# Kernel optimization log

Measured on AMD Instinct MI355X. Metric: run time of the kernel, lower is better.

The kernel has to match this reference:

```python
import jax, jax.numpy as jnp
import numpy as np

M, N_ATOMS, E_MOL, IN_CH, OUT_CH = 10000, 32, 64, 64, 128
HID = 2 * OUT_CH  # 256
E_KG = 320000


def gcn_conv(x, edge_index, W, b):
    # PyG GCNConv: out = D^-1/2 (A+I) D^-1/2 (x W) + b
    N = x.shape[0]
    loops = jnp.arange(N)
    src = jnp.concatenate([edge_index[0], loops])
    dst = jnp.concatenate([edge_index[1], loops])
    deg = jax.ops.segment_sum(jnp.ones_like(dst, dtype=x.dtype), dst, num_segments=N)
    dinv = jnp.where(deg > 0, jax.lax.rsqrt(deg), 0.0)
    norm = dinv[src] * dinv[dst]  # [E+N]
    xw = x @ W  # [N, F_out]
    out = jax.ops.segment_sum(xw[src] * norm[:, None], dst, num_segments=N)
    return out + b


def mol_gnn(mx, mei, W1, b1, W2, b2, W3, b3):
    h = jax.nn.relu(gcn_conv(mx, mei, W1, b1))
    h = jax.nn.relu(gcn_conv(h, mei, W2, b2))
    h = gcn_conv(h, mei, W3, b3)
    return jnp.min(h, axis=0)  # torch.min(dim=0).values


def _glorot(key, shape):
    fan_in, fan_out = shape
    s = jnp.sqrt(6.0 / (fan_in + fan_out))
    return jax.random.uniform(key, shape, jnp.float32, -s, s)


def setup_inputs() -> dict:
    key = jax.random.key(0)
    ks = jax.random.split(key, 16)
    mol_x = jax.random.normal(ks[0], (M, N_ATOMS, IN_CH), jnp.float32)
    mol_edge_index = jax.random.randint(ks[1], (M, 2, E_MOL), 0, N_ATOMS, jnp.int64)
    kg_edge_index = jax.random.randint(ks[2], (2, E_KG), 0, M, jnp.int64)
    return {
        "mol_x": mol_x,
        "mol_edge_index": mol_edge_index,
        "kg_edge_index": kg_edge_index,
        "W1": _glorot(ks[3], (IN_CH, HID)), "b1": jnp.zeros((HID,), jnp.float32),
        "W2": _glorot(ks[4], (HID, HID)), "b2": jnp.zeros((HID,), jnp.float32),
        "W3": _glorot(ks[5], (HID, OUT_CH)), "b3": jnp.zeros((OUT_CH,), jnp.float32),
        "Wk1": _glorot(ks[6], (OUT_CH, HID)), "bk1": jnp.zeros((HID,), jnp.float32),
        "Wk2": _glorot(ks[7], (HID, OUT_CH)), "bk2": jnp.zeros((OUT_CH,), jnp.float32),
    }


def reference(mol_x, mol_edge_index, kg_edge_index, W1, b1, W2, b2, W3, b3, Wk1, bk1, Wk2, bk2):
    # Per-molecule GNN + min-pool, vectorized over the M molecules (each graph is disjoint,
    # so vmap == the original per-graph Python loop)
    embed = jax.vmap(mol_gnn, in_axes=(0, 0, None, None, None, None, None, None))(
        mol_x, mol_edge_index, W1, b1, W2, b2, W3, b3)  # [M, OUT_CH]
    h = jax.nn.relu(gcn_conv(embed, kg_edge_index, Wk1, bk1))
    return gcn_conv(h, kg_edge_index, Wk2, bk2)  # [M, OUT_CH]
```

## Files before the change

kernel.cpp:

```cpp
#include <hip/hip_runtime.h>

#define M_MOLS  10000
#define NA      32
#define E_MOL   64
#define IN_CH   64
#define OUT_CH  128
#define HID     256
#define E_KG    320000
#define KG_N    10000

typedef __attribute__((ext_vector_type(8))) short  s16x8;
typedef __attribute__((ext_vector_type(4))) short  s16x4;
typedef __attribute__((ext_vector_type(4))) float  f32x4;

static __device__ __forceinline__ short f2bf(float f) {
    unsigned u = __float_as_uint(f);
    u += 0x7FFFu + ((u >> 16) & 1u);
    return (short)(u >> 16);
}

__global__ void prep_wt(const float* __restrict__ W, short* __restrict__ WT,
                        int K, int C, int total) {
    int idx = blockIdx.x * 256 + threadIdx.x;
    if (idx < total) {
        int c = idx / K, k = idx - c * K;
        WT[idx] = f2bf(W[k * C + c]);
    }
}

__global__ __launch_bounds__(256, 6) void mol_kernel(
    const float* __restrict__ mol_x, const int* __restrict__ mol_ei,
    const short* __restrict__ WT1, const float* __restrict__ b1,
    const short* __restrict__ WT2, const float* __restrict__ b2,
    const short* __restrict__ WT3, const float* __restrict__ b3,
    float* __restrict__ embed)
{
    __shared__ short Hs[NA * HID];
    __shared__ short BT[NA * 40];
    __shared__ float Bm[NA * NA];
    __shared__ float bias_s[2 * HID + OUT_CH];
    __shared__ int   se[E_MOL], de[E_MOL];
    __shared__ float dinv[NA];
    __shared__ int   deg[NA];

    const int t    = threadIdx.x;
    const int mol  = blockIdx.x;
    const int lane = t & 63;
    const int wid  = t >> 6;
    const int lr   = lane & 15;
    const int lk   = lane >> 4;
    char* HsB = (char*)Hs;

    {
        const float4* src = (const float4*)(mol_x + (size_t)mol * (NA * IN_CH));
        float4 a = src[t * 2], b = src[t * 2 + 1];
        s16x8 v;
        v[0] = f2bf(a.x); v[1] = f2bf(a.y); v[2] = f2bf(a.z); v[3] = f2bf(a.w);
        v[4] = f2bf(b.x); v[5] = f2bf(b.y); v[6] = f2bf(b.z); v[7] = f2bf(b.w);
        int row = t >> 3, k0 = (t & 7) * 8;
        int byte = (row << 9) + (k0 << 1); byte ^= (row & 7) << 4;
        *(s16x8*)(HsB + byte) = v;
    }
    {
        const int* eb = mol_ei + (size_t)mol * (2 * E_MOL);
        if (t < E_MOL)            se[t]         = eb[t];
        else if (t < 2 * E_MOL)   de[t - E_MOL] = eb[t];
    }
    if (t < NA) deg[t] = 1;
    for (int i = t; i < NA * NA; i += 256) Bm[i] = 0.f;
    for (int i = t; i < 2 * HID + OUT_CH; i += 256)
        bias_s[i] = (i < HID) ? b1[i] : (i < 2 * HID) ? b2[i - HID] : b3[i - 2 * HID];
    __syncthreads();
    if (t < E_MOL) atomicAdd(&deg[de[t]], 1);
    __syncthreads();
    if (t < NA) dinv[t] = rsqrtf((float)deg[t]);
    __syncthreads();
    if (t < E_MOL) {
        atomicAdd(&Bm[se[t] * NA + de[t]], dinv[se[t]] * dinv[de[t]]);
    } else if (t < E_MOL + NA) {
        int i = t - E_MOL;
        atomicAdd(&Bm[i * NA + i], dinv[i] * dinv[i]);
    }
    __syncthreads();
    for (int i = t; i < NA * NA; i += 256) {
        int r = i >> 5, s = i & 31;
        BT[r * 40 + s] = f2bf(Bm[s * NA + r]);
    }
    __syncthreads();

    const f32x4 z4 = {0.f, 0.f, 0.f, 0.f};

#define GEMM_PHASE(WT, K, NCT, CT0)                                            \
    _Pragma("unroll")                                                          \
    for (int it = 0; it < 2; ++it)                                             \
        _Pragma("unroll")                                                      \
        for (int c = 0; c < NCT; ++c) acc[it][c] = z4;                         \
    for (int ks = 0; ks < (K) / 32; ++ks) {                                    \
        s16x8 af[2];                                                           \
        _Pragma("unroll")                                                      \
        for (int it = 0; it < 2; ++it) {                                       \
            int row = it * 16 + lr;                                            \
            int byte = (row << 9) + ((ks * 32 + lk * 8) << 1);                 \
            byte ^= (row & 7) << 4;                                            \
            af[it] = *(const s16x8*)(HsB + byte);                              \
        }                                                                      \
        _Pragma("unroll")                                                      \
        for (int c = 0; c < NCT; ++c) {                                        \
            s16x8 bf = *(const s16x8*)((WT) +                                  \
                (size_t)(((CT0) + c) * 16 + lr) * (K) + ks * 32 + lk * 8);     \
            acc[0][c] = __builtin_amdgcn_mfma_f32_16x16x32_bf16(af[0], bf,     \
                                                               acc[0][c], 0, 0, 0); \
            acc[1][c] = __builtin_amdgcn_mfma_f32_16x16x32_bf16(af[1], bf,     \
                                                               acc[1][c], 0, 0, 0); \
        }                                                                      \
    }

#define TRANSPOSE(cIdx, atf)                                                   \
    {                                                                          \
        float vals[8];                                                         \
        _Pragma("unroll")                                                      \
        for (int m = 0; m < 8; ++m) {                                          \
            int src = ((((lk & 1) << 1) + (m >> 2)) << 4) + lr;                \
            float v0 = __shfl(acc[0][cIdx][m & 3], src);                       \
            float v1 = __shfl(acc[1][cIdx][m & 3], src);                       \
            vals[m] = (lk & 2) ? v1 : v0;                                      \
        }                                                                      \
        _Pragma("unroll")                                                      \
        for (int m = 0; m < 8; ++m) atf[m] = f2bf(vals[m]);                    \
    }

#define AGG_PHASE(NCT, CT0, BOFF, RELU)                                        \
    _Pragma("unroll")                                                          \
    for (int c = 0; c < NCT; ++c) {                                            \
        s16x8 atf;                                                             \
        TRANSPOSE(c, atf)                                                      \
        _Pragma("unroll")                                                      \
        for (int itn = 0; itn < 2; ++itn) {                                    \
            s16x8 btf = *(const s16x8*)(BT + (itn * 16 + lr) * 40 + lk * 8);   \
            f32x4 g = __builtin_amdgcn_mfma_f32_16x16x32_bf16(atf, btf, z4,    \
                                                              0, 0, 0);        \
            int c0 = ((CT0) + c) * 16 + lk * 4;                                \
            s16x4 w;                                                           \
            _Pragma("unroll")                                                  \
            for (int jj = 0; jj < 4; ++jj) {                                   \
                float v = g[jj] + bias_s[(BOFF) + c0 + jj];                    \
                if (RELU) v = v > 0.f ? v : 0.f;                               \
                w[jj] = f2bf(v);                                               \
            }                                                                  \
            int row = itn * 16 + lr;                                           \
            int byte = (row << 9) + (c0 << 1); byte ^= (row & 7) << 4;         \
            *(s16x4*)(HsB + byte) = w;                                         \
        }                                                                      \
    }

    const int ct0 = wid * 4;
    const int ct3 = wid * 2;
    {
        f32x4 acc[2][4];
        GEMM_PHASE(WT1, IN_CH, 4, ct0)
        __syncthreads();
        AGG_PHASE(4, ct0, 0, true)
        __syncthreads();
    }
    {
        f32x4 acc[2][4];
        GEMM_PHASE(WT2, HID, 4, ct0)
        __syncthreads();
        AGG_PHASE(4, ct0, HID, true)
        __syncthreads();
    }
    {
        f32x4 acc[2][2];
        GEMM_PHASE(WT3, HID, 2, ct3)
        __syncthreads();
        #pragma unroll
        for (int c = 0; c < 2; ++c) {
            s16x8 atf;
            TRANSPOSE(c, atf)
            float mn[4] = {1e30f, 1e30f, 1e30f, 1e30f};
            #pragma unroll
            for (int itn = 0; itn < 2; ++itn) {
                s16x8 btf = *(const s16x8*)(BT + (itn * 16 + lr) * 40 + lk * 8);
                f32x4 g = __builtin_amdgcn_mfma_f32_16x16x32_bf16(atf, btf, z4,
                                                                  0, 0, 0);
                #pragma unroll
                for (int jj = 0; jj < 4; ++jj) mn[jj] = fminf(mn[jj], g[jj]);
            }
            #pragma unroll
            for (int off = 1; off < 16; off <<= 1) {
                #pragma unroll
                for (int jj = 0; jj < 4; ++jj)
                    mn[jj] = fminf(mn[jj], __shfl_xor(mn[jj], off));
            }
            if (lr == 0) {
                int c0 = (ct3 + c) * 16 + lk * 4;
                #pragma unroll
                for (int jj = 0; jj < 4; ++jj)
                    Bm[c0 + jj] = mn[jj] + bias_s[2 * HID + c0 + jj];
            }
        }
    }
    __syncthreads();
    if (t < OUT_CH) embed[(size_t)mol * OUT_CH + t] = Bm[t];
#undef GEMM_PHASE
#undef TRANSPOSE
#undef AGG_PHASE
}

__global__ void kg_count(const int* __restrict__ kg_ei, int* __restrict__ degi) {
    int e = blockIdx.x * 256 + threadIdx.x;
    if (e < E_KG) atomicAdd(&degi[kg_ei[E_KG + e]], 1);
}

__global__ void kg_dinv(const int* __restrict__ degi, float* __restrict__ dinvk) {
    int i = blockIdx.x * 256 + threadIdx.x;
    if (i < KG_N) dinvk[i] = rsqrtf((float)(degi[i] + 1));
}

__global__ __launch_bounds__(1024) void scan_kernel(const int* __restrict__ degi,
                                                    int* __restrict__ ptr, int n) {
    __shared__ int wsum[16];
    const int t = threadIdx.x;
    const int base = t * 10;
    int inc[10];
    int s = 0;
    #pragma unroll
    for (int i = 0; i < 10; ++i) {
        int idx = base + i;
        s += (idx < n) ? degi[idx] : 0;
        inc[i] = s;
    }
    const int lane = t & 63;
    int ps = s;
    #pragma unroll
    for (int off = 1; off < 64; off <<= 1) {
        int u = __shfl_up(ps, off);
        if (lane >= off) ps += u;
    }
    if (lane == 63) wsum[t >> 6] = ps;
    __syncthreads();
    if (t == 0) {
        int run = 0;
        #pragma unroll
        for (int k = 0; k < 16; ++k) { int x = wsum[k]; wsum[k] = run; run += x; }
        ptr[0] = 0;
    }
    __syncthreads();
    const int excl = wsum[t >> 6] + (ps - s);
    #pragma unroll
    for (int i = 0; i < 10; ++i) {
        int idx = base + i;
        if (idx < n) ptr[idx + 1] = excl + inc[i];
    }
}

__global__ void kg_fill(const int* __restrict__ kg_ei, const int* __restrict__ ptr,
                        int* __restrict__ cursor, int* __restrict__ csr) {
    int e = blockIdx.x * 256 + threadIdx.x;
    if (e < E_KG) {
        int s = kg_ei[e];
        int d = kg_ei[E_KG + e];
        int pos = atomicAdd(&cursor[d], 1);
        csr[ptr[d] + pos] = s;
    }
}

__global__ __launch_bounds__(256) void kg_gemm1(const float* __restrict__ X,
                                                const float* __restrict__ W,
                                                const float* __restrict__ dinvk,
                                                float* __restrict__ Y) {
    __shared__ float es[4 * OUT_CH];
    const int t  = threadIdx.x;
    const int r0 = blockIdx.x * 4;
    if (t < 128) ((float4*)es)[t] = ((const float4*)(X + (size_t)r0 * OUT_CH))[t];
    __syncthreads();
    const int c = t;
    float a0 = 0.f, a1 = 0.f, a2 = 0.f, a3 = 0.f;
    for (int k = 0; k < OUT_CH; k += 4) {
        const float w0 = W[(k + 0) * HID + c], w1 = W[(k + 1) * HID + c],
                    w2 = W[(k + 2) * HID + c], w3 = W[(k + 3) * HID + c];
        float4 e0 = *(const float4*)&es[0 * OUT_CH + k];
        float4 e1 = *(const float4*)&es[1 * OUT_CH + k];
        float4 e2 = *(const float4*)&es[2 * OUT_CH + k];
        float4 e3 = *(const float4*)&es[3 * OUT_CH + k];
        a0 = fmaf(e0.x, w0, fmaf(e0.y, w1, fmaf(e0.z, w2, fmaf(e0.w, w3, a0))));
        a1 = fmaf(e1.x, w0, fmaf(e1.y, w1, fmaf(e1.z, w2, fmaf(e1.w, w3, a1))));
        a2 = fmaf(e2.x, w0, fmaf(e2.y, w1, fmaf(e2.z, w2, fmaf(e2.w, w3, a2))));
        a3 = fmaf(e3.x, w0, fmaf(e3.y, w1, fmaf(e3.z, w2, fmaf(e3.w, w3, a3))));
    }
    Y[(size_t)(r0 + 0) * HID + c] = dinvk[r0 + 0] * a0;
    Y[(size_t)(r0 + 1) * HID + c] = dinvk[r0 + 1] * a1;
    Y[(size_t)(r0 + 2) * HID + c] = dinvk[r0 + 2] * a2;
    Y[(size_t)(r0 + 3) * HID + c] = dinvk[r0 + 3] * a3;
}

__global__ __launch_bounds__(256) void kg_gemm2(const float* __restrict__ X,
                                                const float* __restrict__ W,
                                                const float* __restrict__ dinvk,
                                                float* __restrict__ Y) {
    __shared__ float es[8 * HID];
    const int t  = threadIdx.x;
    const int r0 = blockIdx.x * 8;
    {
        const float4* src = (const float4*)(X + (size_t)r0 * HID);
        float4* dst = (float4*)es;
        dst[t]       = src[t];
        dst[t + 256] = src[t + 256];
    }
    __syncthreads();
    const int c   = t & 127;
    const int rr0 = (t >> 7) * 4;
    float acc[4] = {0.f, 0.f, 0.f, 0.f};
    for (int k = 0; k < HID; k += 4) {
        const float w0 = W[(k + 0) * OUT_CH + c], w1 = W[(k + 1) * OUT_CH + c],
                    w2 = W[(k + 2) * OUT_CH + c], w3 = W[(k + 3) * OUT_CH + c];
        #pragma unroll
        for (int r = 0; r < 4; ++r) {
            float4 e = *(const float4*)&es[(rr0 + r) * HID + k];
            acc[r] = fmaf(e.x, w0, fmaf(e.y, w1, fmaf(e.z, w2, fmaf(e.w, w3, acc[r]))));
        }
    }
    #pragma unroll
    for (int r = 0; r < 4; ++r)
        Y[(size_t)(r0 + rr0 + r) * OUT_CH + c] = dinvk[r0 + rr0 + r] * acc[r];
}

template <int C, bool RELU>
__global__ __launch_bounds__(64) void kg_agg_kernel(
    const float* __restrict__ xw, const float* __restrict__ dinvk,
    const int* __restrict__ ptr, const int* __restrict__ csr,
    const float* __restrict__ bias, float* __restrict__ out)
{
    constexpr int C4  = C / 4;
    constexpr int NPB = 64 / C4;
    const int sub = threadIdx.x / C4;
    const int t   = threadIdx.x - sub * C4;
    const int n   = blockIdx.x * NPB + sub;
    const float4* xw4 = (const float4*)xw;
    const int e1 = ptr[n + 1];
    float4 acc = xw4[(size_t)n * C4 + t];
    for (int e = ptr[n]; e < e1; ++e) {
        int s = csr[e];
        float4 v = xw4[(size_t)s * C4 + t];
        acc.x += v.x; acc.y += v.y; acc.z += v.z; acc.w += v.w;
    }
    const float dn = dinvk[n];
    const float4 b = ((const float4*)bias)[t];
    float4 o;
    o.x = fmaf(dn, acc.x, b.x); o.y = fmaf(dn, acc.y, b.y);
    o.z = fmaf(dn, acc.z, b.z); o.w = fmaf(dn, acc.w, b.w);
    if (RELU) {
        o.x = o.x > 0.f ? o.x : 0.f; o.y = o.y > 0.f ? o.y : 0.f;
        o.z = o.z > 0.f ? o.z : 0.f; o.w = o.w > 0.f ? o.w : 0.f;
    }
    ((float4*)out)[(size_t)n * C4 + t] = o;
}

extern "C" void kernel_launch(void* const* d_in, const int* in_sizes, int n_in,
                              void* d_out, int out_size, void* d_ws, size_t ws_size,
                              hipStream_t stream) {
    const float* mol_x  = (const float*)d_in[0];
    const int*   mol_ei = (const int*)  d_in[1];
    const int*   kg_ei  = (const int*)  d_in[2];
    const float* W1 = (const float*)d_in[3];  const float* b1 = (const float*)d_in[4];
    const float* W2 = (const float*)d_in[5];  const float* b2 = (const float*)d_in[6];
    const float* W3 = (const float*)d_in[7];  const float* b3 = (const float*)d_in[8];
    const float* Wk1 = (const float*)d_in[9];  const float* bk1 = (const float*)d_in[10];
    const float* Wk2 = (const float*)d_in[11]; const float* bk2 = (const float*)d_in[12];
    float* out = (float*)d_out;

    char* ws = (char*)d_ws;
    size_t off = 0;
    auto alloc = [&](size_t bytes) -> void* {
        void* p = ws + off;
        off += (bytes + 255) & ~(size_t)255;
        return p;
    };
    float* embed = (float*)alloc((size_t)M_MOLS * OUT_CH * 4);
    float* xw1   = (float*)alloc((size_t)KG_N * HID * 4);
    float* h1    = (float*)alloc((size_t)KG_N * HID * 4);
    float* xw2   = (float*)alloc((size_t)KG_N * OUT_CH * 4);
    int*   degi  = (int*)  alloc((size_t)KG_N * 4);
    float* dinvk = (float*)alloc((size_t)KG_N * 4);
    int*   ptr   = (int*)  alloc((size_t)(KG_N + 4) * 4);
    int*   cursor= (int*)  alloc((size_t)KG_N * 4);
    int*   csr   = (int*)  alloc((size_t)E_KG * 4);
    short* wt1   = (short*)alloc((size_t)IN_CH * HID * 2);
    short* wt2   = (short*)alloc((size_t)HID * HID * 2);
    short* wt3   = (short*)alloc((size_t)OUT_CH * HID * 2);

    hipMemsetAsync(degi,   0, (size_t)KG_N * 4, stream);
    hipMemsetAsync(cursor, 0, (size_t)KG_N * 4, stream);

    prep_wt<<<(IN_CH * HID + 255) / 256, 256, 0, stream>>>(W1, wt1, IN_CH, HID, IN_CH * HID);
    prep_wt<<<(HID * HID + 255) / 256, 256, 0, stream>>>(W2, wt2, HID, HID, HID * HID);
    prep_wt<<<(OUT_CH * HID + 255) / 256, 256, 0, stream>>>(W3, wt3, HID, OUT_CH, HID * OUT_CH);

    mol_kernel<<<M_MOLS, 256, 0, stream>>>(mol_x, mol_ei, wt1, b1, wt2, b2, wt3, b3, embed);

    kg_count<<<(E_KG + 255) / 256, 256, 0, stream>>>(kg_ei, degi);
    scan_kernel<<<1, 1024, 0, stream>>>(degi, ptr, KG_N);
    kg_dinv<<<(KG_N + 255) / 256, 256, 0, stream>>>(degi, dinvk);
    kg_fill<<<(E_KG + 255) / 256, 256, 0, stream>>>(kg_ei, ptr, cursor, csr);

    kg_gemm1<<<KG_N / 4, 256, 0, stream>>>(embed, Wk1, dinvk, xw1);
    kg_agg_kernel<HID, true><<<KG_N, 64, 0, stream>>>(xw1, dinvk, ptr, csr, bk1, h1);

    kg_gemm2<<<KG_N / 8, 256, 0, stream>>>(h1, Wk2, dinvk, xw2);
    kg_agg_kernel<OUT_CH, false><<<KG_N / 2, 64, 0, stream>>>(xw2, dinvk, ptr, csr, bk2, out);
}
```

Measured before the change: 612.6 us.

## Aggregate before GEMM in first KG layer and fold dinv scaling into mol kernel

The first KG GCN layer is reordered so the normalized neighbour sum is computed on the 128-wide embeddings first (A·X), followed by the GEMM with Wk1 and fused bias+ReLU. The gather therefore moves 128-channel rows instead of 256-channel rows. The source-side dinv scale is applied when mol_kernel writes embed. The molecule adjacency is also built directly in transposed form, which removes a strided transpose pass. mol_kernel's launch-bounds occupancy hint drops from 6 to 4, which may change register allocation.

```diff
diff --git a/kernel.cpp b/kernel.cpp
--- a/kernel.cpp
+++ b/kernel.cpp
@@ -28,16 +28,16 @@
     }
 }
 
-__global__ __launch_bounds__(256, 6) void mol_kernel(
+__global__ __launch_bounds__(256, 4) void mol_kernel(
     const float* __restrict__ mol_x, const int* __restrict__ mol_ei,
     const short* __restrict__ WT1, const float* __restrict__ b1,
     const short* __restrict__ WT2, const float* __restrict__ b2,
     const short* __restrict__ WT3, const float* __restrict__ b3,
-    float* __restrict__ embed)
+    const float* __restrict__ dinvk, float* __restrict__ embed)
 {
     __shared__ short Hs[NA * HID];
     __shared__ short BT[NA * 40];
-    __shared__ float Bm[NA * NA];
+    __shared__ float BmT[NA * NA];
     __shared__ float bias_s[2 * HID + OUT_CH];
     __shared__ int   se[E_MOL], de[E_MOL];
     __shared__ float dinv[NA];
@@ -67,7 +67,7 @@
         else if (t < 2 * E_MOL)   de[t - E_MOL] = eb[t];
     }
     if (t < NA) deg[t] = 1;
-    for (int i = t; i < NA * NA; i += 256) Bm[i] = 0.f;
+    for (int i = t; i < NA * NA; i += 256) BmT[i] = 0.f;
     for (int i = t; i < 2 * HID + OUT_CH; i += 256)
         bias_s[i] = (i < HID) ? b1[i] : (i < 2 * HID) ? b2[i - HID] : b3[i - 2 * HID];
     __syncthreads();
@@ -76,16 +76,14 @@
     if (t < NA) dinv[t] = rsqrtf((float)deg[t]);
     __syncthreads();
     if (t < E_MOL) {
-        atomicAdd(&Bm[se[t] * NA + de[t]], dinv[se[t]] * dinv[de[t]]);
+        atomicAdd(&BmT[de[t] * NA + se[t]], dinv[se[t]] * dinv[de[t]]);
     } else if (t < E_MOL + NA) {
         int i = t - E_MOL;
-        atomicAdd(&Bm[i * NA + i], dinv[i] * dinv[i]);
-    }
-    __syncthreads();
-    for (int i = t; i < NA * NA; i += 256) {
-        int r = i >> 5, s = i & 31;
-        BT[r * 40 + s] = f2bf(Bm[s * NA + r]);
-    }
+        atomicAdd(&BmT[i * NA + i], dinv[i] * dinv[i]);
+    }
+    __syncthreads();
+    for (int i = t; i < NA * NA; i += 256)
+        BT[(i >> 5) * 40 + (i & 31)] = f2bf(BmT[i]);
     __syncthreads();
 
     const f32x4 z4 = {0.f, 0.f, 0.f, 0.f};
@@ -196,12 +194,12 @@
                 int c0 = (ct3 + c) * 16 + lk * 4;
                 #pragma unroll
                 for (int jj = 0; jj < 4; ++jj)
-                    Bm[c0 + jj] = mn[jj] + bias_s[2 * HID + c0 + jj];
+                    BmT[c0 + jj] = mn[jj] + bias_s[2 * HID + c0 + jj];
             }
         }
     }
     __syncthreads();
-    if (t < OUT_CH) embed[(size_t)mol * OUT_CH + t] = Bm[t];
+    if (t < OUT_CH) embed[(size_t)mol * OUT_CH + t] = BmT[t] * dinvk[mol];
 #undef GEMM_PHASE
 #undef TRANSPOSE
 #undef AGG_PHASE
@@ -265,10 +263,39 @@
     }
 }
 
-__global__ __launch_bounds__(256) void kg_gemm1(const float* __restrict__ X,
-                                                const float* __restrict__ W,
-                                                const float* __restrict__ dinvk,
-                                                float* __restrict__ Y) {
+template <bool ADD_BIAS>
+__global__ __launch_bounds__(64) void kg_gather(
+    const float* __restrict__ xs, const float* __restrict__ dinvk,
+    const int* __restrict__ ptr, const int* __restrict__ csr,
+    const float* __restrict__ bias, float* __restrict__ out)
+{
+    const int sub = threadIdx.x >> 5;
+    const int t   = threadIdx.x & 31;
+    const int n   = blockIdx.x * 2 + sub;
+    const float4* x4 = (const float4*)xs;
+    const int e1 = ptr[n + 1];
+    float4 acc = x4[(size_t)n * 32 + t];
+    for (int e = ptr[n]; e < e1; ++e) {
+        int s = csr[e];
+        float4 v = x4[(size_t)s * 32 + t];
+        acc.x += v.x; acc.y += v.y; acc.z += v.z; acc.w += v.w;
+    }
+    const float dn = dinvk[n];
+    float4 o;
+    if (ADD_BIAS) {
+        const float4 b = ((const float4*)bias)[t];
+        o.x = fmaf(dn, acc.x, b.x); o.y = fmaf(dn, acc.y, b.y);
+        o.z = fmaf(dn, acc.z, b.z); o.w = fmaf(dn, acc.w, b.w);
+    } else {
+        o.x = dn * acc.x; o.y = dn * acc.y; o.z = dn * acc.z; o.w = dn * acc.w;
+    }
+    ((float4*)out)[(size_t)n * 32 + t] = o;
+}
+
+__global__ __launch_bounds__(256) void kg_gemm_relu(const float* __restrict__ X,
+                                                    const float* __restrict__ W,
+                                                    const float* __restrict__ bias,
+                                                    float* __restrict__ Y) {
     __shared__ float es[4 * OUT_CH];
     const int t  = threadIdx.x;
     const int r0 = blockIdx.x * 4;
@@ -288,16 +315,18 @@
         a2 = fmaf(e2.x, w0, fmaf(e2.y, w1, fmaf(e2.z, w2, fmaf(e2.w, w3, a2))));
         a3 = fmaf(e3.x, w0, fmaf(e3.y, w1, fmaf(e3.z, w2, fmaf(e3.w, w3, a3))));
     }
-    Y[(size_t)(r0 + 0) * HID + c] = dinvk[r0 + 0] * a0;
-    Y[(size_t)(r0 + 1) * HID + c] = dinvk[r0 + 1] * a1;
-    Y[(size_t)(r0 + 2) * HID + c] = dinvk[r0 + 2] * a2;
-    Y[(size_t)(r0 + 3) * HID + c] = dinvk[r0 + 3] * a3;
-}
-
-__global__ __launch_bounds__(256) void kg_gemm2(const float* __restrict__ X,
-                                                const float* __restrict__ W,
-                                                const float* __restrict__ dinvk,
-                                                float* __restrict__ Y) {
+    const float bc = bias[c];
+    float v0 = a0 + bc, v1 = a1 + bc, v2 = a2 + bc, v3 = a3 + bc;
+    Y[(size_t)(r0 + 0) * HID + c] = v0 > 0.f ? v0 : 0.f;
+    Y[(size_t)(r0 + 1) * HID + c] = v1 > 0.f ? v1 : 0.f;
+    Y[(size_t)(r0 + 2) * HID + c] = v2 > 0.f ? v2 : 0.f;
+    Y[(size_t)(r0 + 3) * HID + c] = v3 > 0.f ? v3 : 0.f;
+}
+
+__global__ __launch_bounds__(256) void kg_gemm_scale(const float* __restrict__ X,
+                                                     const float* __restrict__ W,
+                                                     const float* __restrict__ dinvk,
+                                                     float* __restrict__ Y) {
     __shared__ float es[8 * HID];
     const int t  = threadIdx.x;
     const int r0 = blockIdx.x * 8;
@@ -323,37 +352,6 @@
     #pragma unroll
     for (int r = 0; r < 4; ++r)
         Y[(size_t)(r0 + rr0 + r) * OUT_CH + c] = dinvk[r0 + rr0 + r] * acc[r];
-}
-
-template <int C, bool RELU>
-__global__ __launch_bounds__(64) void kg_agg_kernel(
-    const float* __restrict__ xw, const float* __restrict__ dinvk,
-    const int* __restrict__ ptr, const int* __restrict__ csr,
-    const float* __restrict__ bias, float* __restrict__ out)
-{
-    constexpr int C4  = C / 4;
-    constexpr int NPB = 64 / C4;
-    const int sub = threadIdx.x / C4;
-    const int t   = threadIdx.x - sub * C4;
-    const int n   = blockIdx.x * NPB + sub;
-    const float4* xw4 = (const float4*)xw;
-    const int e1 = ptr[n + 1];
-    float4 acc = xw4[(size_t)n * C4 + t];
-    for (int e = ptr[n]; e < e1; ++e) {
-        int s = csr[e];
-        float4 v = xw4[(size_t)s * C4 + t];
-        acc.x += v.x; acc.y += v.y; acc.z += v.z; acc.w += v.w;
-    }
-    const float dn = dinvk[n];
-    const float4 b = ((const float4*)bias)[t];
-    float4 o;
-    o.x = fmaf(dn, acc.x, b.x); o.y = fmaf(dn, acc.y, b.y);
-    o.z = fmaf(dn, acc.z, b.z); o.w = fmaf(dn, acc.w, b.w);
-    if (RELU) {
-        o.x = o.x > 0.f ? o.x : 0.f; o.y = o.y > 0.f ? o.y : 0.f;
-        o.z = o.z > 0.f ? o.z : 0.f; o.w = o.w > 0.f ? o.w : 0.f;
-    }
-    ((float4*)out)[(size_t)n * C4 + t] = o;
 }
 
 extern "C" void kernel_launch(void* const* d_in, const int* in_sizes, int n_in,
@@ -377,9 +375,9 @@
         return p;
     };
     float* embed = (float*)alloc((size_t)M_MOLS * OUT_CH * 4);
-    float* xw1   = (float*)alloc((size_t)KG_N * HID * 4);
+    float* G     = (float*)alloc((size_t)KG_N * OUT_CH * 4);
     float* h1    = (float*)alloc((size_t)KG_N * HID * 4);
-    float* xw2   = (float*)alloc((size_t)KG_N * OUT_CH * 4);
+    float* xw2s  = (float*)alloc((size_t)KG_N * OUT_CH * 4);
     int*   degi  = (int*)  alloc((size_t)KG_N * 4);
     float* dinvk = (float*)alloc((size_t)KG_N * 4);
     int*   ptr   = (int*)  alloc((size_t)(KG_N + 4) * 4);
@@ -392,20 +390,21 @@
     hipMemsetAsync(degi,   0, (size_t)KG_N * 4, stream);
     hipMemsetAsync(cursor, 0, (size_t)KG_N * 4, stream);
 
-    prep_wt<<<(IN_CH * HID + 255) / 256, 256, 0, stream>>>(W1, wt1, IN_CH, HID, IN_CH * HID);
-    prep_wt<<<(HID * HID + 255) / 256, 256, 0, stream>>>(W2, wt2, HID, HID, HID * HID);
-    prep_wt<<<(OUT_CH * HID + 255) / 256, 256, 0, stream>>>(W3, wt3, HID, OUT_CH, HID * OUT_CH);
-
-    mol_kernel<<<M_MOLS, 256, 0, stream>>>(mol_x, mol_ei, wt1, b1, wt2, b2, wt3, b3, embed);
-
     kg_count<<<(E_KG + 255) / 256, 256, 0, stream>>>(kg_ei, degi);
     scan_kernel<<<1, 1024, 0, stream>>>(degi, ptr, KG_N);
     kg_dinv<<<(KG_N + 255) / 256, 256, 0, stream>>>(degi, dinvk);
     kg_fill<<<(E_KG + 255) / 256, 256, 0, stream>>>(kg_ei, ptr, cursor, csr);
 
-    kg_gemm1<<<KG_N / 4, 256, 0, stream>>>(embed, Wk1, dinvk, xw1);
-    kg_agg_kernel<HID, true><<<KG_N, 64, 0, stream>>>(xw1, dinvk, ptr, csr, bk1, h1);
-
-    kg_gemm2<<<KG_N / 8, 256, 0, stream>>>(h1, Wk2, dinvk, xw2);
-    kg_agg_kernel<OUT_CH, false><<<KG_N / 2, 64, 0, stream>>>(xw2, dinvk, ptr, csr, bk2, out);
-}
+    prep_wt<<<(IN_CH * HID + 255) / 256, 256, 0, stream>>>(W1, wt1, IN_CH, HID, IN_CH * HID);
+    prep_wt<<<(HID * HID + 255) / 256, 256, 0, stream>>>(W2, wt2, HID, HID, HID * HID);
+    prep_wt<<<(OUT_CH * HID + 255) / 256, 256, 0, stream>>>(W3, wt3, HID, OUT_CH, HID * OUT_CH);
+
+    mol_kernel<<<M_MOLS, 256, 0, stream>>>(mol_x, mol_ei, wt1, b1, wt2, b2, wt3, b3,
+                                           dinvk, embed);
+
+    kg_gather<false><<<KG_N / 2, 64, 0, stream>>>(embed, dinvk, ptr, csr, nullptr, G);
+    kg_gemm_relu<<<KG_N / 4, 256, 0, stream>>>(G, Wk1, bk1, h1);
+
+    kg_gemm_scale<<<KG_N / 8, 256, 0, stream>>>(h1, Wk2, dinvk, xw2s);
+    kg_gather<true><<<KG_N / 2, 64, 0, stream>>>(xw2s, dinvk, ptr, csr, bk2, out);
+}
```

Result: faster. 555.2 us (-9.4%).
